# Kernel tuning notes

Measured on AMD Instinct MI355X. Metric: run time of the kernel, lower is better.

The kernel has to match this reference:

```python
import jax, jax.numpy as jnp
import numpy as np

NUM_HEADS = 12
TOP_P = 0.9


def setup_inputs() -> dict:
    key = jax.random.key(0)
    ks = jax.random.split(key, 5)
    B, N, C = 2, 2048, 768
    return {
        "x": jax.random.normal(ks[0], (B, N, C), jnp.float32),
        "qkv_w": jax.random.normal(ks[1], (3 * C, C), jnp.float32) * (C ** -0.5),
        "proj_w": jax.random.normal(ks[2], (C, C), jnp.float32) * (C ** -0.5),
        "proj_b": jax.random.normal(ks[3], (C,), jnp.float32) * 0.02,
        "temperature": jnp.ones((1,), jnp.float32),
        "top_k": 64,
    }


def reference(x, qkv_w, proj_w, proj_b, temperature, top_k):
    B, N, C = x.shape
    H = NUM_HEADS
    D = C // H
    # qkv projection: [B,N,3C] -> [3,B,H,N,D]
    qkv = (x @ qkv_w.T).reshape(B, N, 3, H, D).transpose(2, 0, 3, 1, 4)
    q, k, v = qkv[0], qkv[1], qkv[2]
    scale = (D ** -0.5) * temperature  # (1,) broadcasts
    attn = jnp.einsum("bhnd,bhmd->bhnm", q, k) * scale  # [B,H,N,N]
    neg_inf = jnp.asarray(-jnp.inf, attn.dtype)
    # top-k filtering: keep only scores >= k-th largest per row
    kth = jax.lax.top_k(attn, top_k)[0][..., -1:]
    attn = jnp.where(attn < kth, neg_inf, attn)
    # top-p (nucleus) filtering on sorted scores
    order = jnp.argsort(-attn, axis=-1)  # descending sort indices
    sorted_attn = jnp.take_along_axis(attn, order, axis=-1)
    cum = jnp.cumsum(jax.nn.softmax(sorted_attn, axis=-1), axis=-1)
    rm = cum > TOP_P
    # shift right by one, always keep the top entry
    rm = jnp.concatenate([jnp.zeros_like(rm[..., :1]), rm[..., :-1]], axis=-1)
    # scatter back to original positions via inverse permutation
    inv = jnp.argsort(order, axis=-1)
    remove = jnp.take_along_axis(rm, inv, axis=-1)
    attn = jnp.where(remove, neg_inf, attn)
    p = jax.nn.softmax(attn, axis=-1)
    out = jnp.einsum("bhnm,bhmd->bhnd", p, v)  # [B,H,N,D]
    out = out.transpose(0, 2, 1, 3).reshape(B, N, C)
    return out @ proj_w.T + proj_b
```

## Files before the change

### kernel.cpp

```cpp
#include <hip/hip_runtime.h>
#include <cstdint>

#define NH 12
#define HD 64
#define NSEQ 2048
#define CDIM 768
#define NB 2

__global__ __launch_bounds__(256, 4) void qkv_qk(const float* __restrict__ x,
                                                 const float* __restrict__ w,
                                                 double* __restrict__ Q64,
                                                 double* __restrict__ K64,
                                                 float* __restrict__ Qs32,
                                                 float* __restrict__ Kt32) {
    __shared__ float As[16][128];
    __shared__ float Bs[16][64];
    const int tid = threadIdx.x;
    const int bm = blockIdx.y * 128;
    const int bn = blockIdx.x * 64;
    const int alm = tid >> 1, alk = (tid & 1) * 8;
    const int blm = tid & 63, blk = (tid >> 6) * 4;
    const int tx = tid & 15, ty = tid >> 4;

    double acc[8][4] = {};
    for (int k0 = 0; k0 < CDIM; k0 += 16) {
        float4 a0 = *reinterpret_cast<const float4*>(&x[(bm + alm) * CDIM + k0 + alk]);
        float4 a1 = *reinterpret_cast<const float4*>(&x[(bm + alm) * CDIM + k0 + alk + 4]);
        float4 b0 = *reinterpret_cast<const float4*>(&w[(bn + blm) * CDIM + k0 + blk]);
        __syncthreads();
        As[alk + 0][alm] = a0.x; As[alk + 1][alm] = a0.y;
        As[alk + 2][alm] = a0.z; As[alk + 3][alm] = a0.w;
        As[alk + 4][alm] = a1.x; As[alk + 5][alm] = a1.y;
        As[alk + 6][alm] = a1.z; As[alk + 7][alm] = a1.w;
        Bs[blk + 0][blm] = b0.x; Bs[blk + 1][blm] = b0.y;
        Bs[blk + 2][blm] = b0.z; Bs[blk + 3][blm] = b0.w;
        __syncthreads();
#pragma unroll
        for (int k = 0; k < 16; ++k) {
            float4 af0 = *reinterpret_cast<const float4*>(&As[k][ty * 8]);
            float4 af1 = *reinterpret_cast<const float4*>(&As[k][ty * 8 + 4]);
            float4 bf  = *reinterpret_cast<const float4*>(&Bs[k][tx * 4]);
            double ad[8] = {(double)af0.x, (double)af0.y, (double)af0.z, (double)af0.w,
                            (double)af1.x, (double)af1.y, (double)af1.z, (double)af1.w};
            double bd[4] = {(double)bf.x, (double)bf.y, (double)bf.z, (double)bf.w};
#pragma unroll
            for (int i = 0; i < 8; ++i)
#pragma unroll
                for (int j = 0; j < 4; ++j) acc[i][j] = fma(ad[i], bd[j], acc[i][j]);
        }
        __syncthreads();
    }
    const bool isQ = bn < CDIM;
    const int hh = (isQ ? bn : bn - CDIM) >> 6;
    const int b  = bm >> 11;
    const int bh = b * NH + hh;
#pragma unroll
    for (int i = 0; i < 8; ++i) {
        const int n = (bm + ty * 8 + i) & (NSEQ - 1);
        const size_t base = ((size_t)bh * NSEQ + n) * HD + tx * 4;
        if (isQ) {
            double2 d01; d01.x = acc[i][0]; d01.y = acc[i][1];
            double2 d23; d23.x = acc[i][2]; d23.y = acc[i][3];
            *reinterpret_cast<double2*>(&Q64[base]) = d01;
            *reinterpret_cast<double2*>(&Q64[base + 2]) = d23;
            *reinterpret_cast<float4*>(&Qs32[base]) =
                make_float4((float)acc[i][0], (float)acc[i][1], (float)acc[i][2], (float)acc[i][3]);
        } else {
            double2 d01; d01.x = acc[i][0]; d01.y = acc[i][1];
            double2 d23; d23.x = acc[i][2]; d23.y = acc[i][3];
            *reinterpret_cast<double2*>(&K64[base]) = d01;
            *reinterpret_cast<double2*>(&K64[base + 2]) = d23;
#pragma unroll
            for (int j = 0; j < 4; ++j)
                Kt32[((size_t)bh * HD + tx * 4 + j) * NSEQ + n] = (float)acc[i][j];
        }
    }
}

__global__ __launch_bounds__(256) void qkv_v(const float* __restrict__ x,
                                             const float* __restrict__ wv,
                                             float* __restrict__ V) {
    __shared__ float As[16][64];
    __shared__ float Bs[16][64];
    const int tid = threadIdx.x;
    const int bm = blockIdx.y * 64;
    const int bn = blockIdx.x * 64;
    const int lm = tid >> 2;
    const int lk = (tid & 3) << 2;
    const int tx = tid & 15, ty = tid >> 4;

    float acc[4][4] = {};
    for (int k0 = 0; k0 < CDIM; k0 += 16) {
        float4 av = *reinterpret_cast<const float4*>(&x[(bm + lm) * CDIM + k0 + lk]);
        float4 bv = *reinterpret_cast<const float4*>(&wv[(bn + lm) * CDIM + k0 + lk]);
        __syncthreads();
        As[lk + 0][lm] = av.x; As[lk + 1][lm] = av.y; As[lk + 2][lm] = av.z; As[lk + 3][lm] = av.w;
        Bs[lk + 0][lm] = bv.x; Bs[lk + 1][lm] = bv.y; Bs[lk + 2][lm] = bv.z; Bs[lk + 3][lm] = bv.w;
        __syncthreads();
#pragma unroll
        for (int k = 0; k < 16; ++k) {
            float4 a4 = *reinterpret_cast<const float4*>(&As[k][ty * 4]);
            float4 b4 = *reinterpret_cast<const float4*>(&Bs[k][tx * 4]);
            float aa[4] = {a4.x, a4.y, a4.z, a4.w};
            float bb[4] = {b4.x, b4.y, b4.z, b4.w};
#pragma unroll
            for (int i = 0; i < 4; ++i)
#pragma unroll
                for (int j = 0; j < 4; ++j) acc[i][j] = fmaf(aa[i], bb[j], acc[i][j]);
        }
    }
    const int hh = bn >> 6;
    const int b  = bm >> 11;
#pragma unroll
    for (int i = 0; i < 4; ++i) {
        const int n = (bm + ty * 4 + i) & (NSEQ - 1);
        *reinterpret_cast<float4*>(&V[(((size_t)b * NH + hh) * NSEQ + n) * HD + tx * 4]) =
            make_float4(acc[i][0], acc[i][1], acc[i][2], acc[i][3]);
    }
}

__device__ inline unsigned long long d2key(double f) {
    unsigned long long u = (unsigned long long)__double_as_longlong(f);
    return u ^ (unsigned long long)(((long long)u >> 63) | (long long)0x8000000000000000ull);
}
__device__ inline double key2d(unsigned long long k) {
    unsigned long long mask = ((long long)k < 0) ? 0x8000000000000000ull : 0xFFFFFFFFFFFFFFFFull;
    return __longlong_as_double((long long)(k ^ mask));
}
__device__ inline unsigned kp(float a, float b) {
    unsigned ua = __float_as_uint(a);
    ua ^= (unsigned)(((int)ua >> 31) | 0x80000000);
    unsigned ub = __float_as_uint(b);
    ub ^= (unsigned)(((int)ub >> 31) | 0x80000000);
    return (ua >> 16) | (ub & 0xFFFF0000u);
}

__global__ __launch_bounds__(512, 6) void attn_kernel(const double* __restrict__ Q64,
                                                      const double* __restrict__ K64,
                                                      const float* __restrict__ Qs32,
                                                      const float* __restrict__ Kt32,
                                                      const float* __restrict__ V,
                                                      const float* __restrict__ temp,
                                                      const int* __restrict__ topk_p,
                                                      float* __restrict__ AO) {
    __shared__ unsigned short sk[8][NSEQ];
    __shared__ int cand[8][128];
    __shared__ int cnt8[8];

    const int tid  = threadIdx.x;
    const int bh   = blockIdx.x >> 8;
    const int g0   = (blockIdx.x & 255) << 3;
    const int lane = tid & 63;
    const int wv   = tid >> 6;

    const double scale = 0.125 * (double)temp[0];
    const float sc32 = (float)scale;
    int TK = *topk_p;
    if (TK > 64) TK = 64;
    if (TK < 1)  TK = 1;

    if (tid < 8) cnt8[tid] = 0;
    __syncthreads();

    const float* __restrict__ kb = Kt32 + (size_t)bh * HD * NSEQ;
    const float* __restrict__ qp = Qs32 + ((size_t)bh * NSEQ + g0) * HD;
    const int m0 = tid * 4;
    float acc[8][4] = {};
#pragma unroll 4
    for (int d = 0; d < HD; ++d) {
        float4 k4 = *reinterpret_cast<const float4*>(&kb[(size_t)d * NSEQ + m0]);
        float kv[4] = {k4.x, k4.y, k4.z, k4.w};
#pragma unroll
        for (int r8 = 0; r8 < 8; ++r8) {
            float qv = qp[r8 * HD + d];
#pragma unroll
            for (int c = 0; c < 4; ++c) acc[r8][c] = fmaf(qv, kv[c], acc[r8][c]);
        }
    }
#pragma unroll
    for (int r8 = 0; r8 < 8; ++r8) {
        uint2 pkv;
        pkv.x = kp(acc[r8][0] * sc32, acc[r8][1] * sc32);
        pkv.y = kp(acc[r8][2] * sc32, acc[r8][3] * sc32);
        *reinterpret_cast<uint2*>(&sk[r8][m0]) = pkv;
    }
    __syncthreads();

    const int r = wv;
    const int row = g0 + r;

    int k32[32];
#pragma unroll
    for (int i = 0; i < 32; ++i) k32[i] = sk[r][i * 64 + lane];

    int mx = k32[0];
#pragma unroll
    for (int i = 1; i < 32; ++i) mx = max(mx, k32[i]);
#pragma unroll
    for (int off = 32; off > 0; off >>= 1) mx = max(mx, __shfl_xor(mx, off));

    int lo0 = mx > 1024 ? mx - 1024 : 0;
    int c0 = 0;
#pragma unroll
    for (int i = 0; i < 32; ++i) c0 += (k32[i] >= lo0) ? 1 : 0;
#pragma unroll
    for (int off = 32; off > 0; off >>= 1) c0 += __shfl_xor(c0, off);
    int lo, hi, clo;
    if (c0 >= TK) { lo = lo0; clo = c0; hi = mx; }
    else          { lo = 0;   clo = NSEQ; hi = lo0 - 1; }
    while (lo < hi && clo > 96) {
        int mid = lo + ((hi - lo + 1) >> 1);
        int c = 0;
#pragma unroll
        for (int i = 0; i < 32; ++i) c += (k32[i] >= mid) ? 1 : 0;
#pragma unroll
        for (int off = 32; off > 0; off >>= 1) c += __shfl_xor(c, off);
        if (c >= TK) { lo = mid; clo = c; } else hi = mid - 1;
    }
    int thr = lo >= 2 ? lo - 2 : 0;

#pragma unroll
    for (int i = 0; i < 32; ++i) {
        if (k32[i] >= thr) {
            int slot = atomicAdd(&cnt8[r], 1);
            if (slot < 128) cand[r][slot] = i * 64 + lane;
        }
    }
    asm volatile("s_waitcnt lgkmcnt(0)" ::: "memory");
    int ncand = cnt8[r];
    if (ncand > 128) ncand = 128;

    const int gidx = lane >> 3;
    const int sl   = lane & 7;
    const double* __restrict__ qrow = Q64 + ((size_t)bh * NSEQ + row) * HD;
    double qd[8];
#pragma unroll
    for (int j = 0; j < 8; ++j) qd[j] = qrow[sl * 8 + j];

    unsigned long long* pkr = reinterpret_cast<unsigned long long*>(&sk[r][0]);
    const double* __restrict__ kbase = K64 + (size_t)bh * NSEQ * HD;
#pragma unroll 2
    for (int j = 0; j < 16; ++j) {
        const int s = gidx * 16 + j;
        const int ms = cand[r][min(s, ncand - 1)];
        const double* __restrict__ kp8 = kbase + (size_t)ms * HD + sl * 8;
        double a = 0.0;
#pragma unroll
        for (int d = 0; d < 8; ++d) a = fma(qd[d], kp8[d], a);
        a += __shfl_xor(a, 1);
        a += __shfl_xor(a, 2);
        a += __shfl_xor(a, 4);
        a *= scale;
        unsigned long long pkv = (s < ncand)
            ? ((d2key(a) & ~2047ull) | (unsigned long long)(2047 - ms)) : 0ull;
        if (sl == (j & 7)) pkr[s] = pkv;
    }
    asm volatile("s_waitcnt lgkmcnt(0)" ::: "memory");
    unsigned long long pk1 = pkr[lane];
    unsigned long long pk2 = pkr[64 + lane];

    unsigned long long t0 = ~pk1, t1 = ~pk2;
#pragma unroll
    for (int k = 2; k <= 64; k <<= 1) {
#pragma unroll
        for (int j = k >> 1; j > 0; j >>= 1) {
            {
                unsigned long long ot = __shfl_xor(t0, j);
                bool dir = (lane & k) != 0;
                bool lower = (lane & j) == 0;
                bool takeMin = (lower != dir);
                bool less = t0 < ot;
                t0 = (takeMin == less) ? t0 : ot;
            }
            {
                unsigned long long ot = __shfl_xor(t1, j);
                bool dir = (k == 64) ? true : ((lane & k) != 0);
                bool lower = (lane & j) == 0;
                bool takeMin = (lower != dir);
                bool less = t1 < ot;
                t1 = (takeMin == less) ? t1 : ot;
            }
        }
    }
    {
        unsigned long long na = (t1 < t0) ? t1 : t0;
        unsigned long long nb = (t1 < t0) ? t0 : t1;
        t0 = na; t1 = nb;
    }
#pragma unroll
    for (int j = 32; j > 0; j >>= 1) {
        {
            unsigned long long ot = __shfl_xor(t0, j);
            bool lower = (lane & j) == 0;
            bool less = t0 < ot;
            t0 = (lower == less) ? t0 : ot;
        }
        {
            unsigned long long ot = __shfl_xor(t1, j);
            bool lower = (lane & j) == 0;
            bool less = t1 < ot;
            t1 = (lower == less) ? t1 : ot;
        }
    }
    unsigned long long kk = ~t0;
    int mi = 2047 - (int)(kk & 2047ull);
    bool valid = lane < TK;
    double a = valid ? key2d(kk & ~2047ull) : 0.0;
    double amax = __shfl(a, 0);
    double s = valid ? exp(a - amax) : 0.0;

    double ps = s;
#pragma unroll
    for (int off = 1; off < 64; off <<= 1) {
        double tt = __shfl_up(ps, off);
        if (lane >= off) ps += tt;
    }
    double S = __shfl(ps, 63);
    double cumprev = (ps - s) / S;
    bool keep = valid && ((lane == 0) || (cumprev <= 0.9));
    double sk2 = keep ? s : 0.0;
    double S2 = sk2;
#pragma unroll
    for (int off = 32; off > 0; off >>= 1) S2 += __shfl_xor(S2, off);
    float p = (float)(keep ? (s / S2) : 0.0);

    unsigned long long bal = __ballot(keep);
    int nk = __popcll(bal);

    const float* __restrict__ vb = V + (size_t)bh * NSEQ * HD;
    float o = 0.f;
    for (int i = 0; i < nk; ++i) {
        float pi = __shfl(p, i);
        int midx = __shfl(mi, i);
        o = fmaf(pi, vb[(size_t)midx * HD + lane], o);
    }
    const int b = bh / NH, hh = bh % NH;
    AO[((size_t)b * NSEQ + row) * CDIM + hh * HD + lane] = o;
}

__global__ __launch_bounds__(256) void proj_gemm(const float* __restrict__ A,
                                                 const float* __restrict__ w,
                                                 const float* __restrict__ bias,
                                                 float* __restrict__ out) {
    __shared__ float As[16][64];
    __shared__ float Bs[16][64];
    const int tid = threadIdx.x;
    const int bm = blockIdx.y * 64;
    const int bn = blockIdx.x * 64;
    const int lm = tid >> 2;
    const int lk = (tid & 3) << 2;
    const int tx = tid & 15, ty = tid >> 4;

    float acc[4][4] = {};
    for (int k0 = 0; k0 < CDIM; k0 += 16) {
        float4 av = *reinterpret_cast<const float4*>(&A[(bm + lm) * CDIM + k0 + lk]);
        float4 bv = *reinterpret_cast<const float4*>(&w[(bn + lm) * CDIM + k0 + lk]);
        __syncthreads();
        As[lk + 0][lm] = av.x; As[lk + 1][lm] = av.y; As[lk + 2][lm] = av.z; As[lk + 3][lm] = av.w;
        Bs[lk + 0][lm] = bv.x; Bs[lk + 1][lm] = bv.y; Bs[lk + 2][lm] = bv.z; Bs[lk + 3][lm] = bv.w;
        __syncthreads();
#pragma unroll
        for (int k = 0; k < 16; ++k) {
            float4 a4 = *reinterpret_cast<const float4*>(&As[k][ty * 4]);
            float4 b4 = *reinterpret_cast<const float4*>(&Bs[k][tx * 4]);
            float aa[4] = {a4.x, a4.y, a4.z, a4.w};
            float bb[4] = {b4.x, b4.y, b4.z, b4.w};
#pragma unroll
            for (int i = 0; i < 4; ++i)
#pragma unroll
                for (int j = 0; j < 4; ++j) acc[i][j] = fmaf(aa[i], bb[j], acc[i][j]);
        }
    }
    float4 bv = *reinterpret_cast<const float4*>(&bias[bn + tx * 4]);
#pragma unroll
    for (int i = 0; i < 4; ++i) {
        int r = bm + ty * 4 + i;
        float4 v4 = make_float4(acc[i][0] + bv.x, acc[i][1] + bv.y,
                                acc[i][2] + bv.z, acc[i][3] + bv.w);
        *reinterpret_cast<float4*>(&out[(size_t)r * CDIM + bn + tx * 4]) = v4;
    }
}

extern "C" void kernel_launch(void* const* d_in, const int* in_sizes, int n_in,
                              void* d_out, int out_size, void* d_ws, size_t ws_size,
                              hipStream_t stream) {
    const float* x      = (const float*)d_in[0];
    const float* qkv_w  = (const float*)d_in[1];
    const float* proj_w = (const float*)d_in[2];
    const float* proj_b = (const float*)d_in[3];
    const float* temp   = (const float*)d_in[4];
    const int*   topk   = (const int*)d_in[5];
    float* out = (float*)d_out;

    const size_t HSZ = (size_t)NB * NH * NSEQ * HD;
    double* Q64  = (double*)d_ws;
    double* K64  = Q64 + HSZ;
    float*  Qs32 = (float*)(K64 + HSZ);
    float*  Kt32 = Qs32 + HSZ;
    float*  V    = Kt32 + HSZ;
    float*  AO   = V + HSZ;

    qkv_qk<<<dim3(24, 32), 256, 0, stream>>>(x, qkv_w, Q64, K64, Qs32, Kt32);
    qkv_v<<<dim3(12, 64), 256, 0, stream>>>(x, qkv_w + (size_t)2 * CDIM * CDIM, V);
    attn_kernel<<<dim3(NB * NH * (NSEQ / 8)), 512, 0, stream>>>(Q64, K64, Qs32, Kt32, V, temp, topk, AO);
    proj_gemm<<<dim3(12, 64), 256, 0, stream>>>(AO, proj_w, proj_b, out);
}
```

Measured before the change: 816.0 us.

## Tune GEMM tiles, replace atomic candidate compaction with ballots, stagger K loads

The QKV GEMM now converts its inputs to double once when staging them in shared memory, instead of converting on every inner-loop read. This doubles the LDS footprint of that kernel. The attention kernel's top-k threshold search now counts with ballot/popcount rather than shuffle reductions, and builds the candidate list with a ballot-prefix compaction in place of shared atomics. It also rotates the per-group iteration order of the K64 gather, intended to spread memory and LDS accesses. The projection GEMM moves to 128x64 tiles with 8x4 outputs per thread, halving its grid and adding a trailing barrier.

```diff
diff --git a/kernel.cpp b/kernel.cpp
--- a/kernel.cpp
+++ b/kernel.cpp
@@ -13,8 +13,8 @@
                                                  double* __restrict__ K64,
                                                  float* __restrict__ Qs32,
                                                  float* __restrict__ Kt32) {
-    __shared__ float As[16][128];
-    __shared__ float Bs[16][64];
+    __shared__ double As[16][128];
+    __shared__ double Bs[16][64];
     const int tid = threadIdx.x;
     const int bm = blockIdx.y * 128;
     const int bn = blockIdx.x * 64;
@@ -28,21 +28,20 @@
         float4 a1 = *reinterpret_cast<const float4*>(&x[(bm + alm) * CDIM + k0 + alk + 4]);
         float4 b0 = *reinterpret_cast<const float4*>(&w[(bn + blm) * CDIM + k0 + blk]);
         __syncthreads();
-        As[alk + 0][alm] = a0.x; As[alk + 1][alm] = a0.y;
-        As[alk + 2][alm] = a0.z; As[alk + 3][alm] = a0.w;
-        As[alk + 4][alm] = a1.x; As[alk + 5][alm] = a1.y;
-        As[alk + 6][alm] = a1.z; As[alk + 7][alm] = a1.w;
-        Bs[blk + 0][blm] = b0.x; Bs[blk + 1][blm] = b0.y;
-        Bs[blk + 2][blm] = b0.z; Bs[blk + 3][blm] = b0.w;
+        As[alk + 0][alm] = (double)a0.x; As[alk + 1][alm] = (double)a0.y;
+        As[alk + 2][alm] = (double)a0.z; As[alk + 3][alm] = (double)a0.w;
+        As[alk + 4][alm] = (double)a1.x; As[alk + 5][alm] = (double)a1.y;
+        As[alk + 6][alm] = (double)a1.z; As[alk + 7][alm] = (double)a1.w;
+        Bs[blk + 0][blm] = (double)b0.x; Bs[blk + 1][blm] = (double)b0.y;
+        Bs[blk + 2][blm] = (double)b0.z; Bs[blk + 3][blm] = (double)b0.w;
         __syncthreads();
 #pragma unroll
         for (int k = 0; k < 16; ++k) {
-            float4 af0 = *reinterpret_cast<const float4*>(&As[k][ty * 8]);
-            float4 af1 = *reinterpret_cast<const float4*>(&As[k][ty * 8 + 4]);
-            float4 bf  = *reinterpret_cast<const float4*>(&Bs[k][tx * 4]);
-            double ad[8] = {(double)af0.x, (double)af0.y, (double)af0.z, (double)af0.w,
-                            (double)af1.x, (double)af1.y, (double)af1.z, (double)af1.w};
-            double bd[4] = {(double)bf.x, (double)bf.y, (double)bf.z, (double)bf.w};
+            double ad[8], bd[4];
+#pragma unroll
+            for (int i = 0; i < 8; ++i) ad[i] = As[k][ty * 8 + i];
+#pragma unroll
+            for (int j = 0; j < 4; ++j) bd[j] = Bs[k][tx * 4 + j];
 #pragma unroll
             for (int i = 0; i < 8; ++i)
 #pragma unroll
@@ -145,7 +144,6 @@
                                                       float* __restrict__ AO) {
     __shared__ unsigned short sk[8][NSEQ];
     __shared__ int cand[8][128];
-    __shared__ int cnt8[8];
 
     const int tid  = threadIdx.x;
     const int bh   = blockIdx.x >> 8;
@@ -158,9 +156,6 @@
     int TK = *topk_p;
     if (TK > 64) TK = 64;
     if (TK < 1)  TK = 1;
-
-    if (tid < 8) cnt8[tid] = 0;
-    __syncthreads();
 
     const float* __restrict__ kb = Kt32 + (size_t)bh * HD * NSEQ;
     const float* __restrict__ qp = Qs32 + ((size_t)bh * NSEQ + g0) * HD;
@@ -202,9 +197,7 @@
     int lo0 = mx > 1024 ? mx - 1024 : 0;
     int c0 = 0;
 #pragma unroll
-    for (int i = 0; i < 32; ++i) c0 += (k32[i] >= lo0) ? 1 : 0;
-#pragma unroll
-    for (int off = 32; off > 0; off >>= 1) c0 += __shfl_xor(c0, off);
+    for (int i = 0; i < 32; ++i) c0 += (int)__popcll(__ballot(k32[i] >= lo0));
     int lo, hi, clo;
     if (c0 >= TK) { lo = lo0; clo = c0; hi = mx; }
     else          { lo = 0;   clo = NSEQ; hi = lo0 - 1; }
@@ -212,23 +205,25 @@
         int mid = lo + ((hi - lo + 1) >> 1);
         int c = 0;
 #pragma unroll
-        for (int i = 0; i < 32; ++i) c += (k32[i] >= mid) ? 1 : 0;
-#pragma unroll
-        for (int off = 32; off > 0; off >>= 1) c += __shfl_xor(c, off);
+        for (int i = 0; i < 32; ++i) c += (int)__popcll(__ballot(k32[i] >= mid));
         if (c >= TK) { lo = mid; clo = c; } else hi = mid - 1;
     }
     int thr = lo >= 2 ? lo - 2 : 0;
 
+    const unsigned long long lmask = (1ull << lane) - 1ull;
+    int base = 0;
 #pragma unroll
     for (int i = 0; i < 32; ++i) {
-        if (k32[i] >= thr) {
-            int slot = atomicAdd(&cnt8[r], 1);
+        bool pred = k32[i] >= thr;
+        unsigned long long bal = __ballot(pred);
+        if (pred) {
+            int slot = base + (int)__popcll(bal & lmask);
             if (slot < 128) cand[r][slot] = i * 64 + lane;
         }
-    }
+        base += (int)__popcll(bal);
+    }
+    int ncand = min(base, 128);
     asm volatile("s_waitcnt lgkmcnt(0)" ::: "memory");
-    int ncand = cnt8[r];
-    if (ncand > 128) ncand = 128;
 
     const int gidx = lane >> 3;
     const int sl   = lane & 7;
@@ -240,7 +235,8 @@
     unsigned long long* pkr = reinterpret_cast<unsigned long long*>(&sk[r][0]);
     const double* __restrict__ kbase = K64 + (size_t)bh * NSEQ * HD;
 #pragma unroll 2
-    for (int j = 0; j < 16; ++j) {
+    for (int jj = 0; jj < 16; ++jj) {
+        const int j = (jj + gidx) & 15;
         const int s = gidx * 16 + j;
         const int ms = cand[r][min(s, ncand - 1)];
         const double* __restrict__ kp8 = kbase + (size_t)ms * HD + sl * 8;
@@ -253,7 +249,7 @@
         a *= scale;
         unsigned long long pkv = (s < ncand)
             ? ((d2key(a) & ~2047ull) | (unsigned long long)(2047 - ms)) : 0ull;
-        if (sl == (j & 7)) pkr[s] = pkv;
+        if (sl == (jj & 7)) pkr[s] = pkv;
     }
     asm volatile("s_waitcnt lgkmcnt(0)" ::: "memory");
     unsigned long long pk1 = pkr[lane];
@@ -342,42 +338,49 @@
                                                  const float* __restrict__ w,
                                                  const float* __restrict__ bias,
                                                  float* __restrict__ out) {
-    __shared__ float As[16][64];
+    __shared__ float As[16][128];
     __shared__ float Bs[16][64];
     const int tid = threadIdx.x;
-    const int bm = blockIdx.y * 64;
+    const int bm = blockIdx.y * 128;
     const int bn = blockIdx.x * 64;
-    const int lm = tid >> 2;
-    const int lk = (tid & 3) << 2;
+    const int alm = tid >> 1, alk = (tid & 1) * 8;
+    const int blm = tid & 63, blk = (tid >> 6) * 4;
     const int tx = tid & 15, ty = tid >> 4;
 
-    float acc[4][4] = {};
+    float acc[8][4] = {};
     for (int k0 = 0; k0 < CDIM; k0 += 16) {
-        float4 av = *reinterpret_cast<const float4*>(&A[(bm + lm) * CDIM + k0 + lk]);
-        float4 bv = *reinterpret_cast<const float4*>(&w[(bn + lm) * CDIM + k0 + lk]);
-        __syncthreads();
-        As[lk + 0][lm] = av.x; As[lk + 1][lm] = av.y; As[lk + 2][lm] = av.z; As[lk + 3][lm] = av.w;
-        Bs[lk + 0][lm] = bv.x; Bs[lk + 1][lm] = bv.y; Bs[lk + 2][lm] = bv.z; Bs[lk + 3][lm] = bv.w;
+        float4 a0 = *reinterpret_cast<const float4*>(&A[(bm + alm) * CDIM + k0 + alk]);
+        float4 a1 = *reinterpret_cast<const float4*>(&A[(bm + alm) * CDIM + k0 + alk + 4]);
+        float4 b0 = *reinterpret_cast<const float4*>(&w[(bn + blm) * CDIM + k0 + blk]);
+        __syncthreads();
+        As[alk + 0][alm] = a0.x; As[alk + 1][alm] = a0.y;
+        As[alk + 2][alm] = a0.z; As[alk + 3][alm] = a0.w;
+        As[alk + 4][alm] = a1.x; As[alk + 5][alm] = a1.y;
+        As[alk + 6][alm] = a1.z; As[alk + 7][alm] = a1.w;
+        Bs[blk + 0][blm] = b0.x; Bs[blk + 1][blm] = b0.y;
+        Bs[blk + 2][blm] = b0.z; Bs[blk + 3][blm] = b0.w;
         __syncthreads();
 #pragma unroll
         for (int k = 0; k < 16; ++k) {
-            float4 a4 = *reinterpret_cast<const float4*>(&As[k][ty * 4]);
-            float4 b4 = *reinterpret_cast<const float4*>(&Bs[k][tx * 4]);
-            float aa[4] = {a4.x, a4.y, a4.z, a4.w};
-            float bb[4] = {b4.x, b4.y, b4.z, b4.w};
-#pragma unroll
-            for (int i = 0; i < 4; ++i)
+            float4 af0 = *reinterpret_cast<const float4*>(&As[k][ty * 8]);
+            float4 af1 = *reinterpret_cast<const float4*>(&As[k][ty * 8 + 4]);
+            float4 bf  = *reinterpret_cast<const float4*>(&Bs[k][tx * 4]);
+            float aa[8] = {af0.x, af0.y, af0.z, af0.w, af1.x, af1.y, af1.z, af1.w};
+            float bb[4] = {bf.x, bf.y, bf.z, bf.w};
+#pragma unroll
+            for (int i = 0; i < 8; ++i)
 #pragma unroll
                 for (int j = 0; j < 4; ++j) acc[i][j] = fmaf(aa[i], bb[j], acc[i][j]);
         }
+        __syncthreads();
     }
     float4 bv = *reinterpret_cast<const float4*>(&bias[bn + tx * 4]);
 #pragma unroll
-    for (int i = 0; i < 4; ++i) {
-        int r = bm + ty * 4 + i;
+    for (int i = 0; i < 8; ++i) {
+        int rr = bm + ty * 8 + i;
         float4 v4 = make_float4(acc[i][0] + bv.x, acc[i][1] + bv.y,
                                 acc[i][2] + bv.z, acc[i][3] + bv.w);
-        *reinterpret_cast<float4*>(&out[(size_t)r * CDIM + bn + tx * 4]) = v4;
+        *reinterpret_cast<float4*>(&out[(size_t)rr * CDIM + bn + tx * 4]) = v4;
     }
 }
 
@@ -403,5 +406,5 @@
     qkv_qk<<<dim3(24, 32), 256, 0, stream>>>(x, qkv_w, Q64, K64, Qs32, Kt32);
     qkv_v<<<dim3(12, 64), 256, 0, stream>>>(x, qkv_w + (size_t)2 * CDIM * CDIM, V);
     attn_kernel<<<dim3(NB * NH * (NSEQ / 8)), 512, 0, stream>>>(Q64, K64, Qs32, Kt32, V, temp, topk, AO);
-    proj_gemm<<<dim3(12, 64), 256, 0, stream>>>(AO, proj_w, proj_b, out);
-}
+    proj_gemm<<<dim3(12, 32), 256, 0, stream>>>(AO, proj_w, proj_b, out);
+}
```

New measurement: 790.9 us. 1.03x faster.
